# Kernel tuning notes

Hardware: AMD Instinct MI355X
Metric: run time of the kernel (lower is better)

## Reference

```python
import jax, jax.numpy as jnp
import numpy as np

B, NF, NU = 8, 64, 1024
DF, DU, DH, H = 64, 32, 128, 8


def setup_inputs() -> dict:
    key = jax.random.key(0)
    ks = jax.random.split(key, 10)
    s = 0.05  # keep logits in a stable range
    return {
        "f0": jax.random.normal(ks[0], (B, NF, DF), jnp.float32),
        "u0": jax.random.normal(ks[1], (B, NU, DU), jnp.float32),
        "f1": jax.random.normal(ks[2], (B, NF, DF), jnp.float32),
        "u1": jax.random.normal(ks[3], (B, NU, DU), jnp.float32),
        "Wf": jax.random.normal(ks[4], (H, 2, 3, DF, DH), jnp.float32) * s,
        "bf": jax.random.normal(ks[5], (H, 2, 3, DH), jnp.float32) * s,
        "Wu": jax.random.normal(ks[6], (H, 2, 3, DU, DH), jnp.float32) * s,
        "bu": jax.random.normal(ks[7], (H, 2, 3, DH), jnp.float32) * s,
        "Wout": jax.random.normal(ks[8], (H * DH, DH), jnp.float32) * s,
        "bout": jax.random.normal(ks[9], (DH,), jnp.float32) * s,
    }


def _proj(x, W, b):
    # x: [B,N,Din], W: [H,3,Din,DH], b: [H,3,DH] -> [3,B,H,N,DH] (qkv-major)
    y = jnp.einsum('bnf,hkfd->kbhnd', x, W)
    return y + b.transpose(1, 0, 2)[:, None, :, None, :]


def reference(f0, u0, f1, u1, Wf, bf, Wu, bu, Wout, bout):
    # per-head per-player Q/K/V projections; concat order: [f0, u0, f1, u1]
    parts = [
        _proj(f0, Wf[:, 0], bf[:, 0]),
        _proj(u0, Wu[:, 0], bu[:, 0]),
        _proj(f1, Wf[:, 1], bf[:, 1]),
        _proj(u1, Wu[:, 1], bu[:, 1]),
    ]
    qkv = jnp.concatenate(parts, axis=3)  # [3,B,H,S,DH]
    Q, K, V = qkv[0], qkv[1], qkv[2]
    scale = jnp.asarray(DH ** 0.5, Q.dtype)
    scores = jnp.einsum('bhqd,bhkd->bhqk', Q, K) / scale  # [B,H,S,S]
    attn = jax.nn.softmax(scores, axis=-1)
    out = jnp.einsum('bhqk,bhkd->bhqd', attn, V)  # [B,H,S,DH]
    # concat heads along feature dim (head order preserved), then final linear
    S = out.shape[2]
    out = out.transpose(0, 2, 1, 3).reshape(out.shape[0], S, H * DH)
    return out @ Wout + bout  # [B,S,DH]
```

## Files before the change

kernel.cpp:

```cpp
#include <hip/hip_runtime.h>
#include <hip/hip_bf16.h>

#define BB 8
#define NFQ 64
#define NUQ 1024
#define HH 8
#define SS 2176

typedef __attribute__((ext_vector_type(8))) short short8;
typedef __attribute__((ext_vector_type(4))) float f32x4;
typedef __attribute__((ext_vector_type(2))) unsigned int uint2_t;
typedef unsigned short ubf;

__device__ __forceinline__ ubf f2bf(float x) {
    unsigned u = __float_as_uint(x);
    u = u + 0x7fffu + ((u >> 16) & 1u);
    return (ubf)(u >> 16);
}
__device__ __forceinline__ unsigned pkbf(float a, float b) {
    __hip_bfloat162 h = __float22bfloat162_rn(make_float2(a, b));
    union { __hip_bfloat162 hh; unsigned u; } c; c.hh = h;
    return c.u;
}
__device__ __forceinline__ float bf2f(short v) {
    return __uint_as_float(((unsigned)(ubf)v) << 16);
}

__global__ __launch_bounds__(256) void prep_kernel(
    const float* __restrict__ Wf, const float* __restrict__ Wu, const float* __restrict__ Wout,
    ubf* __restrict__ WfT, ubf* __restrict__ WuT, ubf* __restrict__ WoutT)
{
    __shared__ ubf tl[128 * 72];
    const int idx = blockIdx.x, tid = threadIdx.x;
    const float* src; ubf* dst; int F, dstride;
    if (idx < 48)       { F = 64; src = Wf + (size_t)idx * 64 * 128;        dst = WfT + (size_t)idx * 128 * 64;        dstride = 64; }
    else if (idx < 96)  { F = 32; src = Wu + (size_t)(idx - 48) * 32 * 128; dst = WuT + (size_t)(idx - 48) * 128 * 32; dstride = 32; }
    else                { F = 64; int s = idx - 96; src = Wout + (size_t)s * 64 * 128; dst = WoutT + s * 64; dstride = 1024; }
    const int pitch = F + 8;
    for (int i = tid; i < F * 32; i += 256) {
        int f = i >> 5, d0 = (i & 31) * 4;
        f32x4 v = *(const f32x4*)&src[f * 128 + d0];
        tl[(d0 + 0) * pitch + f] = f2bf(v[0]);
        tl[(d0 + 1) * pitch + f] = f2bf(v[1]);
        tl[(d0 + 2) * pitch + f] = f2bf(v[2]);
        tl[(d0 + 3) * pitch + f] = f2bf(v[3]);
    }
    __syncthreads();
    if (F == 64) {
        int d = tid >> 1, half = tid & 1;
#pragma unroll
        for (int jj = 0; jj < 4; ++jj)
            *(short8*)&dst[(size_t)d * dstride + half * 32 + jj * 8] =
                *(const short8*)&tl[d * pitch + half * 32 + jj * 8];
    } else {
        int d = tid & 127, fh = tid >> 7;
#pragma unroll
        for (int jj = 0; jj < 2; ++jj)
            *(short8*)&dst[(size_t)d * dstride + fh * 16 + jj * 8] =
                *(const short8*)&tl[d * pitch + fh * 16 + jj * 8];
    }
}

__global__ __launch_bounds__(256) void proj_kernel(
    const float* __restrict__ f0, const float* __restrict__ u0,
    const float* __restrict__ f1, const float* __restrict__ u1,
    const ubf* __restrict__ WfT, const ubf* __restrict__ WuT,
    const float* __restrict__ bfv, const float* __restrict__ buv,
    ubf* __restrict__ Qg, ubf* __restrict__ Kg, ubf* __restrict__ Vtg)
{
    __shared__ ubf xlds[32 * 64];
    __shared__ ubf outq[32 * 136];
    __shared__ ubf outk[32 * 136];
    __shared__ ubf outv[128 * 40];

    const int tid = threadIdx.x;
    const int bh = blockIdx.x / 17, j = blockIdx.x % 17;
    const int b = bh >> 3, h = bh & 7;
    const int w = tid >> 6, l = tid & 63, lg = l >> 4, dl = l & 15;
    const int dg0 = w * 2;

    const bool isF = (j == 0);
    const f32x4 zf = {0.f, 0.f, 0.f, 0.f};

    short8 af[3][2][2];
    f32x4 bv[3][2];

    const int up = isF ? 0 : ((j - 1) >> 3);
    const int ugrp = isF ? 0 : ((j - 1) & 7);
    const float* xpb = 0;
    if (!isF) xpb = (up ? u1 : u0) + (size_t)b * NUQ * 32;

    for (int c4 = 0; c4 < 4; ++c4) {
        int p, n0, s0;
        const float* xp;
        if (isF) {
            p = c4 >> 1; n0 = (c4 & 1) * 32;
            s0 = p ? 1088 + (c4 & 1) * 32 : (c4 & 1) * 32;
            xp = (p ? f1 : f0) + (size_t)b * NFQ * 64;
        } else {
            p = up; int c = ugrp * 4 + c4; n0 = 32 * c;
            s0 = (p ? 1152 : 64) + 32 * c;
            xp = xpb;
        }

        if (c4 == 0 || (isF && c4 == 2)) {
            if (isF) {
                const ubf* wt = WfT + (size_t)((h * 2 + p) * 3) * 8192;
#pragma unroll
                for (int k = 0; k < 3; ++k)
#pragma unroll
                    for (int g = 0; g < 2; ++g) {
                        af[k][g][0] = *(const short8*)&wt[(size_t)k * 8192 + ((dg0 + g) * 16 + dl) * 64 + lg * 8];
                        af[k][g][1] = *(const short8*)&wt[(size_t)k * 8192 + ((dg0 + g) * 16 + dl) * 64 + 32 + lg * 8];
                        bv[k][g] = *(const f32x4*)&bfv[((h * 2 + p) * 3 + k) * 128 + (dg0 + g) * 16 + 4 * lg];
                    }
            } else {
                const ubf* wt = WuT + (size_t)((h * 2 + p) * 3) * 4096;
#pragma unroll
                for (int k = 0; k < 3; ++k)
#pragma unroll
                    for (int g = 0; g < 2; ++g) {
                        af[k][g][0] = *(const short8*)&wt[(size_t)k * 4096 + ((dg0 + g) * 16 + dl) * 32 + lg * 8];
                        bv[k][g] = *(const f32x4*)&buv[((h * 2 + p) * 3 + k) * 128 + (dg0 + g) * 16 + 4 * lg];
                    }
            }
        }

        if (isF) {
            int row = tid >> 3, g = tid & 7;
            const float* s = &xp[(size_t)(n0 + row) * 64 + g * 8];
            f32x4 v0 = *(const f32x4*)&s[0];
            f32x4 v1 = *(const f32x4*)&s[4];
            union { unsigned u[4]; short8 s8; } pk;
            pk.u[0] = pkbf(v0[0], v0[1]); pk.u[1] = pkbf(v0[2], v0[3]);
            pk.u[2] = pkbf(v1[0], v1[1]); pk.u[3] = pkbf(v1[2], v1[3]);
            *(short8*)&xlds[row * 64 + ((g ^ (row & 7)) * 8)] = pk.s8;
        } else if (tid < 128) {
            int row = tid >> 2, g = tid & 3;
            const float* s = &xp[(size_t)(n0 + row) * 32 + g * 8];
            f32x4 v0 = *(const f32x4*)&s[0];
            f32x4 v1 = *(const f32x4*)&s[4];
            union { unsigned u[4]; short8 s8; } pk;
            pk.u[0] = pkbf(v0[0], v0[1]); pk.u[1] = pkbf(v0[2], v0[3]);
            pk.u[2] = pkbf(v1[0], v1[1]); pk.u[3] = pkbf(v1[2], v1[3]);
            *(short8*)&xlds[row * 64 + ((g ^ (row & 7)) * 8)] = pk.s8;
        }
        __syncthreads();

        short8 bx0[2], bx1[2];
#pragma unroll
        for (int tile = 0; tile < 2; ++tile) {
            const int row = tile * 16 + dl;
            bx0[tile] = *(const short8*)&xlds[row * 64 + ((lg ^ (row & 7)) * 8)];
            if (isF)
                bx1[tile] = *(const short8*)&xlds[row * 64 + (((4 + lg) ^ (row & 7)) * 8)];
        }

#pragma unroll
        for (int k = 0; k < 3; ++k)
#pragma unroll
            for (int g = 0; g < 2; ++g)
#pragma unroll
                for (int tile = 0; tile < 2; ++tile) {
                    f32x4 acc = __builtin_amdgcn_mfma_f32_16x16x32_bf16(af[k][g][0], bx0[tile], zf, 0, 0, 0);
                    if (isF)
                        acc = __builtin_amdgcn_mfma_f32_16x16x32_bf16(af[k][g][1], bx1[tile], acc, 0, 0, 0);
                    if (k < 2) {
                        ubf* o = k ? outk : outq;
                        uint2_t wv;
                        wv.x = pkbf(acc[0] + bv[k][g][0], acc[1] + bv[k][g][1]);
                        wv.y = pkbf(acc[2] + bv[k][g][2], acc[3] + bv[k][g][3]);
                        *(uint2_t*)&o[(tile * 16 + dl) * 136 + (dg0 + g) * 16 + 4 * lg] = wv;
                    } else {
                        int pos = (dl & 3) + 8 * ((dl >> 2) & 3) + 4 * tile;
#pragma unroll
                        for (int r = 0; r < 4; ++r)
                            outv[((dg0 + g) * 16 + 4 * lg + r) * 40 + pos] = f2bf(acc[r] + bv[2][g][r]);
                    }
                }
        __syncthreads();

        {
            int row = tid >> 3, c16 = (tid & 7) * 16;
            size_t qbase = ((size_t)bh * SS + s0 + row) * 128 + c16;
            *(short8*)&Qg[qbase]     = *(const short8*)&outq[row * 136 + c16];
            *(short8*)&Qg[qbase + 8] = *(const short8*)&outq[row * 136 + c16 + 8];
            *(short8*)&Kg[qbase]     = *(const short8*)&outk[row * 136 + c16];
            *(short8*)&Kg[qbase + 8] = *(const short8*)&outk[row * 136 + c16 + 8];
            int dd = tid >> 1, half = tid & 1;
            size_t vbase = ((size_t)bh * 128 + dd) * SS + s0 + half * 16;
            *(short8*)&Vtg[vbase]     = *(const short8*)&outv[dd * 40 + half * 16];
            *(short8*)&Vtg[vbase + 8] = *(const short8*)&outv[dd * 40 + half * 16 + 8];
        }
    }
}

__global__ __launch_bounds__(256) void attn_kernel(
    const ubf* __restrict__ Qg, const ubf* __restrict__ Kg, const ubf* __restrict__ Vtg,
    ubf* __restrict__ attnout)
{
    __shared__ ubf Klds[2][32 * 128];
    __shared__ ubf Vlds[2][128 * 40];

    const int tid = threadIdx.x;
    const int swz = (blockIdx.x & 7) * 136 + (blockIdx.x >> 3);
    const int bh = swz / 17;
    const int qc = swz % 17;
    const int b = bh >> 3, h = bh & 7;
    const int w = tid >> 6, l = tid & 63, lg = l >> 4, dl = l & 15;
    const int qr0 = qc * 128 + w * 32 + dl;

    const ubf* Qbh = Qg + (size_t)bh * SS * 128;
    const ubf* Kbh = Kg + (size_t)bh * SS * 128;
    const ubf* Vbh = Vtg + (size_t)bh * 128 * SS;

    short8 qfa[4], qfb[4];
#pragma unroll
    for (int dc = 0; dc < 4; ++dc) {
        qfa[dc] = *(const short8*)&Qbh[(size_t)qr0 * 128 + dc * 32 + lg * 8];
        qfb[dc] = *(const short8*)&Qbh[(size_t)(qr0 + 16) * 128 + dc * 32 + lg * 8];
    }

    f32x4 otA[8], otB[8];
    const f32x4 zf = {0.f, 0.f, 0.f, 0.f};
#pragma unroll
    for (int i = 0; i < 8; ++i) { otA[i] = zf; otB[i] = zf; }
    float lsA = 0.f, lsB = 0.f;

    const int skrow = tid >> 3, skc = tid & 7;
    const int svrow = tid >> 1, svh = tid & 1;
    const float sc = 0.08838834764831845f * 1.44269504088896340736f;

    short8 kst0, kst1, vst0, vst1;
    const ubf* kp = &Kbh[(size_t)skrow * 128 + skc * 16];
    const ubf* vp = &Vbh[(size_t)svrow * SS + svh * 16];
    const int ksw = (skrow & 7) << 3;
    const int ko0 = skrow * 128 + ((skc * 16) ^ ksw);
    const int ko1 = skrow * 128 + ((skc * 16 + 8) ^ ksw);
    const int vo  = svrow * 40 + svh * 16;

    kst0 = *(const short8*)&kp[0];
    kst1 = *(const short8*)&kp[8];
    vst0 = *(const short8*)&vp[0];
    vst1 = *(const short8*)&vp[8];
    *(short8*)&Klds[0][ko0]    = kst0;
    *(short8*)&Klds[0][ko1]    = kst1;
    *(short8*)&Vlds[0][vo]     = vst0;
    *(short8*)&Vlds[0][vo + 8] = vst1;
    __syncthreads();

    int cur = 0;
    for (int it = 0; it < 68; ++it) {
        if (it < 67) {
            const int nb = (it + 1) * 32;
            kst0 = *(const short8*)&kp[(size_t)nb * 128];
            kst1 = *(const short8*)&kp[(size_t)nb * 128 + 8];
            vst0 = *(const short8*)&vp[nb];
            vst1 = *(const short8*)&vp[nb + 8];
        }
        const ubf* Kc = Klds[cur];
        const ubf* Vc = Vlds[cur];

        f32x4 s0a = zf, s1a = zf, s0b = zf, s1b = zf;
        __builtin_amdgcn_s_setprio(1);
#pragma unroll
        for (int dc = 0; dc < 4; ++dc) {
            const int col = (dc * 32 + lg * 8) ^ ((dl & 7) << 3);
            short8 k0 = *(const short8*)&Kc[dl * 128 + col];
            short8 k1 = *(const short8*)&Kc[(16 + dl) * 128 + col];
            s0a = __builtin_amdgcn_mfma_f32_16x16x32_bf16(k0, qfa[dc], s0a, 0, 0, 0);
            s1a = __builtin_amdgcn_mfma_f32_16x16x32_bf16(k1, qfa[dc], s1a, 0, 0, 0);
            s0b = __builtin_amdgcn_mfma_f32_16x16x32_bf16(k0, qfb[dc], s0b, 0, 0, 0);
            s1b = __builtin_amdgcn_mfma_f32_16x16x32_bf16(k1, qfb[dc], s1b, 0, 0, 0);
        }
        __builtin_amdgcn_s_setprio(0);

        float pa[8], pb[8];
#pragma unroll
        for (int r = 0; r < 4; ++r) {
            pa[r]     = __builtin_amdgcn_exp2f(s0a[r] * sc);
            pa[4 + r] = __builtin_amdgcn_exp2f(s1a[r] * sc);
            pb[r]     = __builtin_amdgcn_exp2f(s0b[r] * sc);
            pb[4 + r] = __builtin_amdgcn_exp2f(s1b[r] * sc);
        }
        lsA += ((pa[0]+pa[1]) + (pa[2]+pa[3])) + ((pa[4]+pa[5]) + (pa[6]+pa[7]));
        lsB += ((pb[0]+pb[1]) + (pb[2]+pb[3])) + ((pb[4]+pb[5]) + (pb[6]+pb[7]));

        union { unsigned u[4]; short8 s; } Pa, Pb;
        Pa.u[0] = pkbf(pa[0], pa[1]); Pa.u[1] = pkbf(pa[2], pa[3]);
        Pa.u[2] = pkbf(pa[4], pa[5]); Pa.u[3] = pkbf(pa[6], pa[7]);
        Pb.u[0] = pkbf(pb[0], pb[1]); Pb.u[1] = pkbf(pb[2], pb[3]);
        Pb.u[2] = pkbf(pb[4], pb[5]); Pb.u[3] = pkbf(pb[6], pb[7]);

        __builtin_amdgcn_s_setprio(1);
#pragma unroll
        for (int dt = 0; dt < 8; ++dt) {
            short8 vf = *(const short8*)&Vc[(dt * 16 + dl) * 40 + lg * 8];
            otA[dt] = __builtin_amdgcn_mfma_f32_16x16x32_bf16(vf, Pa.s, otA[dt], 0, 0, 0);
            otB[dt] = __builtin_amdgcn_mfma_f32_16x16x32_bf16(vf, Pb.s, otB[dt], 0, 0, 0);
        }
        __builtin_amdgcn_s_setprio(0);

        if (it < 67) {
            ubf* Kn = Klds[cur ^ 1];
            ubf* Vn = Vlds[cur ^ 1];
            *(short8*)&Kn[ko0]    = kst0;
            *(short8*)&Kn[ko1]    = kst1;
            *(short8*)&Vn[vo]     = vst0;
            *(short8*)&Vn[vo + 8] = vst1;
            cur ^= 1;
            __syncthreads();
        }
    }

    lsA += __shfl_xor(lsA, 16); lsA += __shfl_xor(lsA, 32);
    lsB += __shfl_xor(lsB, 16); lsB += __shfl_xor(lsB, 32);
    const float invA = 1.f / lsA, invB = 1.f / lsB;

    ubf* dstA = attnout + ((size_t)b * SS + qr0) * 1024 + h * 128;
    ubf* dstB = attnout + ((size_t)b * SS + qr0 + 16) * 1024 + h * 128;
#pragma unroll
    for (int dt = 0; dt < 8; ++dt) {
        f32x4 oA = otA[dt] * invA;
        f32x4 oB = otB[dt] * invB;
        uint2_t wA, wB;
        wA.x = pkbf(oA[0], oA[1]); wA.y = pkbf(oA[2], oA[3]);
        wB.x = pkbf(oB[0], oB[1]); wB.y = pkbf(oB[2], oB[3]);
        *(uint2_t*)&dstA[dt * 16 + 4 * lg] = wA;
        *(uint2_t*)&dstB[dt * 16 + 4 * lg] = wB;
    }
}

__global__ __launch_bounds__(256) void outproj_kernel(
    const ubf* __restrict__ attnout, const ubf* __restrict__ WoutT,
    const float* __restrict__ bout, float* __restrict__ out)
{
    __shared__ ubf alds[32 * 1024];
    const int tid = threadIdx.x;
    const int row0 = blockIdx.x * 32;
    const int w = tid >> 6, l = tid & 63, lg = l >> 4, dl = l & 15;
    const int dg0 = w * 2;
    const f32x4 zf = {0.f, 0.f, 0.f, 0.f};

#pragma unroll
    for (int pz = 0; pz < 2; ++pz) {
        int row = pz * 16 + (tid >> 4);
        int cl = tid & 15;
#pragma unroll
        for (int jj = 0; jj < 8; ++jj) {
            int g = cl + 16 * jj;
            short8 v = *(const short8*)&attnout[(size_t)(row0 + row) * 1024 + g * 8];
            *(short8*)&alds[row * 1024 + ((g ^ (row & 7)) * 8)] = v;
        }
    }
    __syncthreads();

    f32x4 acc[2][2];
    acc[0][0] = zf; acc[0][1] = zf; acc[1][0] = zf; acc[1][1] = zf;

    for (int dc = 0; dc < 32; ++dc) {
        short8 a0 = *(const short8*)&WoutT[(size_t)((dg0 + 0) * 16 + dl) * 1024 + dc * 32 + lg * 8];
        short8 a1 = *(const short8*)&WoutT[(size_t)((dg0 + 1) * 16 + dl) * 1024 + dc * 32 + lg * 8];
        short8 b0 = *(const short8*)&alds[dl * 1024 + (((dc * 4 + lg) ^ (dl & 7)) * 8)];
        short8 b1 = *(const short8*)&alds[(16 + dl) * 1024 + (((dc * 4 + lg) ^ (dl & 7)) * 8)];
        acc[0][0] = __builtin_amdgcn_mfma_f32_16x16x32_bf16(a0, b0, acc[0][0], 0, 0, 0);
        acc[0][1] = __builtin_amdgcn_mfma_f32_16x16x32_bf16(a0, b1, acc[0][1], 0, 0, 0);
        acc[1][0] = __builtin_amdgcn_mfma_f32_16x16x32_bf16(a1, b0, acc[1][0], 0, 0, 0);
        acc[1][1] = __builtin_amdgcn_mfma_f32_16x16x32_bf16(a1, b1, acc[1][1], 0, 0, 0);
    }

#pragma unroll
    for (int g = 0; g < 2; ++g) {
        f32x4 bb = *(const f32x4*)&bout[(dg0 + g) * 16 + 4 * lg];
#pragma unroll
        for (int tile = 0; tile < 2; ++tile) {
            f32x4 o = acc[g][tile] + bb;
            *(f32x4*)&out[((size_t)row0 + tile * 16 + dl) * 128 + (dg0 + g) * 16 + 4 * lg] = o;
        }
    }
}

extern "C" void kernel_launch(void* const* d_in, const int* in_sizes, int n_in,
                              void* d_out, int out_size, void* d_ws, size_t ws_size,
                              hipStream_t stream) {
    const float* f0  = (const float*)d_in[0];
    const float* u0  = (const float*)d_in[1];
    const float* f1  = (const float*)d_in[2];
    const float* u1  = (const float*)d_in[3];
    const float* Wf  = (const float*)d_in[4];
    const float* bfv = (const float*)d_in[5];
    const float* Wu  = (const float*)d_in[6];
    const float* buv = (const float*)d_in[7];
    const float* Wout = (const float*)d_in[8];
    const float* bout = (const float*)d_in[9];
    float* out = (float*)d_out;

    char* ws = (char*)d_ws;
    const size_t qkv_bytes = (size_t)BB * HH * SS * 128 * sizeof(ubf);
    ubf* Qg  = (ubf*)ws;
    ubf* Kg  = (ubf*)(ws + qkv_bytes);
    ubf* Vtg = (ubf*)(ws + 2 * qkv_bytes);
    ubf* attnout = (ubf*)(ws + 3 * qkv_bytes);
    ubf* WfT   = (ubf*)(ws + 4 * qkv_bytes);
    ubf* WuT   = (ubf*)(ws + 4 * qkv_bytes + 786432);
    ubf* WoutT = (ubf*)(ws + 4 * qkv_bytes + 786432 + 393216);

    prep_kernel<<<dim3(112), dim3(256), 0, stream>>>(Wf, Wu, Wout, WfT, WuT, WoutT);
    proj_kernel<<<dim3(64 * 17), dim3(256), 0, stream>>>(f0, u0, f1, u1, WfT, WuT, bfv, buv, Qg, Kg, Vtg);
    attn_kernel<<<dim3(64 * 17), dim3(256), 0, stream>>>(Qg, Kg, Vtg, attnout);
    outproj_kernel<<<dim3(544), dim3(256), 0, stream>>>(attnout, WoutT, bout, out);
}
```

Baseline: 306.2 us.

## Double attention block to 8 waves sharing each K/V tile

```diff
diff --git a/kernel.cpp b/kernel.cpp
--- a/kernel.cpp
+++ b/kernel.cpp
@@ -195,7 +195,7 @@
     }
 }
 
-__global__ __launch_bounds__(256) void attn_kernel(
+__global__ __launch_bounds__(512) void attn_kernel(
     const ubf* __restrict__ Qg, const ubf* __restrict__ Kg, const ubf* __restrict__ Vtg,
     ubf* __restrict__ attnout)
 {
@@ -203,12 +203,15 @@
     __shared__ ubf Vlds[2][128 * 40];
 
     const int tid = threadIdx.x;
-    const int swz = (blockIdx.x & 7) * 136 + (blockIdx.x >> 3);
-    const int bh = swz / 17;
-    const int qc = swz % 17;
+    const int swz = (blockIdx.x & 7) * 72 + (blockIdx.x >> 3);
+    const int bh = swz / 9;
+    const int qc = swz % 9;
     const int b = bh >> 3, h = bh & 7;
     const int w = tid >> 6, l = tid & 63, lg = l >> 4, dl = l & 15;
-    const int qr0 = qc * 128 + w * 32 + dl;
+    int qbase = qc * 256 + w * 32;
+    const bool qvalid = qbase < SS;
+    if (!qvalid) qbase = SS - 32;
+    const int qr0 = qbase + dl;
 
     const ubf* Qbh = Qg + (size_t)bh * SS * 128;
     const ubf* Kbh = Kg + (size_t)bh * SS * 128;
@@ -227,36 +230,28 @@
     for (int i = 0; i < 8; ++i) { otA[i] = zf; otB[i] = zf; }
     float lsA = 0.f, lsB = 0.f;
 
-    const int skrow = tid >> 3, skc = tid & 7;
-    const int svrow = tid >> 1, svh = tid & 1;
+    const int skrow = tid >> 4, skc = tid & 15;
+    const int svrow = tid >> 2, svc = tid & 3;
     const float sc = 0.08838834764831845f * 1.44269504088896340736f;
 
-    short8 kst0, kst1, vst0, vst1;
-    const ubf* kp = &Kbh[(size_t)skrow * 128 + skc * 16];
-    const ubf* vp = &Vbh[(size_t)svrow * SS + svh * 16];
-    const int ksw = (skrow & 7) << 3;
-    const int ko0 = skrow * 128 + ((skc * 16) ^ ksw);
-    const int ko1 = skrow * 128 + ((skc * 16 + 8) ^ ksw);
-    const int vo  = svrow * 40 + svh * 16;
-
-    kst0 = *(const short8*)&kp[0];
-    kst1 = *(const short8*)&kp[8];
-    vst0 = *(const short8*)&vp[0];
-    vst1 = *(const short8*)&vp[8];
-    *(short8*)&Klds[0][ko0]    = kst0;
-    *(short8*)&Klds[0][ko1]    = kst1;
-    *(short8*)&Vlds[0][vo]     = vst0;
-    *(short8*)&Vlds[0][vo + 8] = vst1;
+    short8 kst, vst;
+    const ubf* kp = &Kbh[(size_t)skrow * 128 + skc * 8];
+    const ubf* vp = &Vbh[(size_t)svrow * SS + svc * 8];
+    const int ko = skrow * 128 + ((skc * 8) ^ ((skrow & 7) << 3));
+    const int vo = svrow * 40 + svc * 8;
+
+    kst = *(const short8*)&kp[0];
+    vst = *(const short8*)&vp[0];
+    *(short8*)&Klds[0][ko] = kst;
+    *(short8*)&Vlds[0][vo] = vst;
     __syncthreads();
 
     int cur = 0;
     for (int it = 0; it < 68; ++it) {
         if (it < 67) {
             const int nb = (it + 1) * 32;
-            kst0 = *(const short8*)&kp[(size_t)nb * 128];
-            kst1 = *(const short8*)&kp[(size_t)nb * 128 + 8];
-            vst0 = *(const short8*)&vp[nb];
-            vst1 = *(const short8*)&vp[nb + 8];
+            kst = *(const short8*)&kp[(size_t)nb * 128];
+            vst = *(const short8*)&vp[nb];
         }
         const ubf* Kc = Klds[cur];
         const ubf* Vc = Vlds[cur];
@@ -304,30 +299,30 @@
         if (it < 67) {
             ubf* Kn = Klds[cur ^ 1];
             ubf* Vn = Vlds[cur ^ 1];
-            *(short8*)&Kn[ko0]    = kst0;
-            *(short8*)&Kn[ko1]    = kst1;
-            *(short8*)&Vn[vo]     = vst0;
-            *(short8*)&Vn[vo + 8] = vst1;
+            *(short8*)&Kn[ko] = kst;
+            *(short8*)&Vn[vo] = vst;
             cur ^= 1;
             __syncthreads();
         }
     }
 
-    lsA += __shfl_xor(lsA, 16); lsA += __shfl_xor(lsA, 32);
-    lsB += __shfl_xor(lsB, 16); lsB += __shfl_xor(lsB, 32);
-    const float invA = 1.f / lsA, invB = 1.f / lsB;
-
-    ubf* dstA = attnout + ((size_t)b * SS + qr0) * 1024 + h * 128;
-    ubf* dstB = attnout + ((size_t)b * SS + qr0 + 16) * 1024 + h * 128;
-#pragma unroll
-    for (int dt = 0; dt < 8; ++dt) {
-        f32x4 oA = otA[dt] * invA;
-        f32x4 oB = otB[dt] * invB;
-        uint2_t wA, wB;
-        wA.x = pkbf(oA[0], oA[1]); wA.y = pkbf(oA[2], oA[3]);
-        wB.x = pkbf(oB[0], oB[1]); wB.y = pkbf(oB[2], oB[3]);
-        *(uint2_t*)&dstA[dt * 16 + 4 * lg] = wA;
-        *(uint2_t*)&dstB[dt * 16 + 4 * lg] = wB;
+    if (qvalid) {
+        lsA += __shfl_xor(lsA, 16); lsA += __shfl_xor(lsA, 32);
+        lsB += __shfl_xor(lsB, 16); lsB += __shfl_xor(lsB, 32);
+        const float invA = 1.f / lsA, invB = 1.f / lsB;
+
+        ubf* dstA = attnout + ((size_t)b * SS + qr0) * 1024 + h * 128;
+        ubf* dstB = attnout + ((size_t)b * SS + qr0 + 16) * 1024 + h * 128;
+#pragma unroll
+        for (int dt = 0; dt < 8; ++dt) {
+            f32x4 oA = otA[dt] * invA;
+            f32x4 oB = otB[dt] * invB;
+            uint2_t wA, wB;
+            wA.x = pkbf(oA[0], oA[1]); wA.y = pkbf(oA[2], oA[3]);
+            wB.x = pkbf(oB[0], oB[1]); wB.y = pkbf(oB[2], oB[3]);
+            *(uint2_t*)&dstA[dt * 16 + 4 * lg] = wA;
+            *(uint2_t*)&dstB[dt * 16 + 4 * lg] = wB;
+        }
     }
 }
 
@@ -407,6 +402,6 @@
 
     prep_kernel<<<dim3(112), dim3(256), 0, stream>>>(Wf, Wu, Wout, WfT, WuT, WoutT);
     proj_kernel<<<dim3(64 * 17), dim3(256), 0, stream>>>(f0, u0, f1, u1, WfT, WuT, bfv, buv, Qg, Kg, Vtg);
-    attn_kernel<<<dim3(64 * 17), dim3(256), 0, stream>>>(Qg, Kg, Vtg, attnout);
+    attn_kernel<<<dim3(576), dim3(512), 0, stream>>>(Qg, Kg, Vtg, attnout);
     outproj_kernel<<<dim3(544), dim3(256), 0, stream>>>(attnout, WoutT, bout, out);
 }
```

After: 290.9 us. -5.0%, faster.
